# Kernel optimization log

Hardware: AMD Instinct MI355X
Metric: run time of the kernel (lower is better)

The kernel has to match this reference:

```python
import jax, jax.numpy as jnp
import numpy as np

N = 100000
E = 1600000
IN_F = 128
OUT_F = 32
HEADS = 6
NEG_SLOPE = 0.2


def setup_inputs() -> dict:
    key = jax.random.key(0)
    k1, k2, k3, k4, k5 = jax.random.split(key, 5)
    x = jax.random.normal(k1, (N, IN_F), dtype=jnp.float32)
    edge_index = jax.random.randint(k2, (2, E), 0, N, dtype=jnp.int64)
    # GATConv params (PyG layout): shared linear for src/dst, per-head attention vectors, bias
    glorot = lambda k, shape: jax.random.normal(k, shape, dtype=jnp.float32) * np.sqrt(2.0 / (shape[0] + shape[-1]))
    W = glorot(k3, (IN_F, HEADS * OUT_F))          # lin.weight^T
    att_src = glorot(k4, (HEADS, OUT_F)) * 0.1     # [H, C]
    att_dst = glorot(k5, (HEADS, OUT_F)) * 0.1
    bias = jnp.zeros((OUT_F,), dtype=jnp.float32)  # concat=False -> bias of size out_feature
    return {"x": x, "edge_index": edge_index, "W": W,
            "att_src": att_src, "att_dst": att_dst, "bias": bias}


def reference(x, edge_index, W, att_src, att_dst, bias):
    src, dst = edge_index[0], edge_index[1]
    # Linear projection to per-head features: [N, H, C]
    xp = (x @ W).reshape(N, HEADS, OUT_F)
    # Per-node attention logit halves: [N, H]
    a_s = jnp.einsum("nhc,hc->nh", xp, att_src)
    a_d = jnp.einsum("nhc,hc->nh", xp, att_dst)
    # Per-edge logits with LeakyReLU: [E, H]
    e = jax.nn.leaky_relu(a_s[src] + a_d[dst], negative_slope=NEG_SLOPE)
    # Segment softmax over edges grouped by destination node
    m = jax.ops.segment_max(e, dst, num_segments=N)            # [N, H]
    m = jnp.where(jnp.isfinite(m), m, 0.0)                     # empty segments -> -inf guard
    e = jnp.exp(e - m[dst])
    s = jax.ops.segment_sum(e, dst, num_segments=N)            # [N, H]
    alpha = e / (s[dst] + 1e-16)                               # [E, H]
    # Weighted scatter-add aggregation: [N, H, C]
    msg = xp[src] * alpha[:, :, None]
    out = jax.ops.segment_sum(msg, dst, num_segments=N)
    # concat=False -> mean over heads, add bias, then SELU
    out = out.mean(axis=1) + bias
    return jax.nn.selu(out)
```

## Files before the change

kernel.cpp:

```cpp
#include <hip/hip_runtime.h>


typedef __attribute__((ext_vector_type(8))) short short8;
typedef __attribute__((ext_vector_type(4))) float f32x4;

#define SK 136
#define SLOTS 48

__device__ __forceinline__ unsigned short f2bf(float f)
{
    unsigned int u = __float_as_uint(f);
    u = (u + 0x7fffu + ((u >> 16) & 1u)) >> 16;
    return (unsigned short)u;
}

__global__ __launch_bounds__(256) void k_prep(
    const float* __restrict__ W,
    const float* __restrict__ att_src, const float* __restrict__ att_dst,
    unsigned short* __restrict__ watT, unsigned short* __restrict__ WbT,
    int* __restrict__ deg, int N)
{
    int i = blockIdx.x * 256 + threadIdx.x;
    if (i < N) deg[i] = 0;
    if (i < 128 * 192) {
        int k = i / 192, c = i - k * 192;
        WbT[c * 128 + k] = f2bf(W[i]);
    }
    if (i < 128 * 16) {
        int k = i >> 4, c = i & 15;
        float v = 0.f;
        if (c < 12) {
            int h = c < 6 ? c : c - 6;
            const float* av = (c < 6 ? att_src : att_dst) + h * 32;
            const float* wr = W + k * 192 + h * 32;
            #pragma unroll
            for (int j = 0; j < 32; ++j) v = fmaf(wr[j], av[j], v);
        }
        watT[c * 128 + k] = f2bf(v);
    }
}

__global__ __launch_bounds__(384) void k_gd(
    const float* __restrict__ x, const unsigned short* __restrict__ WbT,
    const unsigned short* __restrict__ watT,
    unsigned char* __restrict__ xpb, float2* __restrict__ asc,
    float* __restrict__ a_d,
    const int* __restrict__ ei, int* __restrict__ deg, int* __restrict__ csr,
    int N, int E, int GB, int DB)
{
    __shared__ __align__(16) unsigned short xt[64 * SK];
    const int t   = threadIdx.x;
    const int bid = (int)blockIdx.x >> 1;

    if (blockIdx.x & 1) {
        if (bid >= DB) return;
        const int G = DB * 384;
        const int gid = bid * 384 + t;
        int s[4], d[4], r[4];
        #pragma unroll
        for (int k = 0; k < 4; ++k) {
            int e = gid + k * G;
            bool ok = e < E;
            int ec = ok ? e : 0;
            s[k] = ei[ec];
            d[k] = ei[E + ec];
            if (!ok) d[k] = -1;
        }
        #pragma unroll
        for (int k = 0; k < 4; ++k)
            r[k] = (d[k] >= 0) ? atomicAdd(&deg[d[k]], 1) : SLOTS;
        #pragma unroll
        for (int k = 0; k < 4; ++k)
            if (r[k] < SLOTS && d[k] >= 0) csr[d[k] * SLOTS + r[k]] = s[k];
        return;
    }

    if (bid >= GB) return;
    const int wave = t >> 6;
    const int lane = t & 63;
    const int ln   = lane & 15;
    const int q    = lane >> 4;
    const int n0   = bid * 64;
    const int cb   = wave * 32;

    {
        const float4* x4 = (const float4*)x;
        #pragma unroll
        for (int it = 0; it < 6; ++it) {
            int i = t + it * 384;
            if (i < 2048) {
                int row = i >> 5;
                int c4  = i & 31;
                int gr  = n0 + row;
                if (gr > N - 1) gr = N - 1;
                float4 f = x4[(size_t)gr * 32 + c4];
                unsigned int u0 = (unsigned int)f2bf(f.x) | ((unsigned int)f2bf(f.y) << 16);
                unsigned int u1 = (unsigned int)f2bf(f.z) | ((unsigned int)f2bf(f.w) << 16);
                *(uint2*)(xt + row * SK + c4 * 4) = make_uint2(u0, u1);
            }
        }
    }

    short8 bw[2][4];
    #pragma unroll
    for (int nt = 0; nt < 2; ++nt)
        #pragma unroll
        for (int kbi = 0; kbi < 4; ++kbi)
            bw[nt][kbi] = *(const short8*)(WbT + (cb + nt * 16 + ln) * 128
                                               + kbi * 32 + q * 8);
    short8 bwa[4];
    if (wave < 4) {
        #pragma unroll
        for (int kbi = 0; kbi < 4; ++kbi)
            bwa[kbi] = *(const short8*)(watT + ln * 128 + kbi * 32 + q * 8);
    }

    __syncthreads();

    f32x4 acc[4][2];
    #pragma unroll
    for (int mt = 0; mt < 4; ++mt)
        #pragma unroll
        for (int nt = 0; nt < 2; ++nt) acc[mt][nt] = (f32x4)0.f;

    #pragma unroll
    for (int kbi = 0; kbi < 4; ++kbi) {
        #pragma unroll
        for (int mt = 0; mt < 4; ++mt) {
            short8 av = *(const short8*)(xt + (mt * 16 + ln) * SK + kbi * 32 + q * 8);
            #pragma unroll
            for (int nt = 0; nt < 2; ++nt)
                acc[mt][nt] = __builtin_amdgcn_mfma_f32_16x16x32_bf16(
                    av, bw[nt][kbi], acc[mt][nt], 0, 0, 0);
        }
    }

    if (wave < 4) {
        f32x4 acca = (f32x4)0.f;
        #pragma unroll
        for (int kbi = 0; kbi < 4; ++kbi) {
            short8 av = *(const short8*)(xt + (wave * 16 + ln) * SK + kbi * 32 + q * 8);
            acca = __builtin_amdgcn_mfma_f32_16x16x32_bf16(av, bwa[kbi], acca, 0, 0, 0);
        }
        #pragma unroll
        for (int r = 0; r < 4; ++r) {
            int grow = n0 + wave * 16 + q * 4 + r;
            if (grow < N) {
                if (ln < 6)       asc[(size_t)grow * 6 + ln].x   = acca[r];
                else if (ln < 12) a_d[(size_t)grow * 6 + ln - 6] = acca[r];
            }
        }
    }

    #pragma unroll
    for (int mt = 0; mt < 4; ++mt) {
        #pragma unroll
        for (int r = 0; r < 4; ++r) {
            float m = fmaxf(fabsf(acc[mt][0][r]), fabsf(acc[mt][1][r]));
            #pragma unroll
            for (int d = 1; d <= 8; d <<= 1)
                m = fmaxf(m, __shfl_xor(m, d));
            int row  = mt * 16 + q * 4 + r;
            int grow = n0 + row;
            if (grow < N) {
                float inv = m > 0.f ? 127.f / m : 0.f;
                if (ln == 0) asc[(size_t)grow * 6 + wave].y = m * (1.f / 127.f);
                #pragma unroll
                for (int nt = 0; nt < 2; ++nt) {
                    int qv = (int)rintf(acc[mt][nt][r] * inv) + 128;
                    xpb[(size_t)grow * 192 + cb + nt * 16 + ln] = (unsigned char)qv;
                }
            }
        }
    }
}

__global__ __launch_bounds__(256) void k_agg(
    const unsigned char* __restrict__ xpb, const float2* __restrict__ asc,
    const float* __restrict__ a_d,
    const int* __restrict__ csr, const int* __restrict__ degv,
    const float* __restrict__ bias, float* __restrict__ out, int N)
{
    const int wid = threadIdx.x >> 6;
    const int l   = threadIdx.x & 63;
    const int n = blockIdx.x * 4 + wid;
    if (n >= N) return;

    int deg = degv[n];
    deg = deg < SLOTS ? deg : SLOTS;
    const int nb  = n * SLOTS;
    const int eh  = l >> 5;
    const int sl0 = l & 31;
    const int sl  = sl0 < 24 ? sl0 : 23;
    const int h   = sl >> 2;
    const unsigned slb = (unsigned)sl * 8u;
    const unsigned h8  = (unsigned)h * 8u;
    const char* __restrict__ xpB  = (const char*)xpb;
    const char* __restrict__ ascB = (const char*)asc;

    const float zd = a_d[(size_t)n * 6 + h];

    float a0 = 0.f, a1 = 0.f, a2 = 0.f, a3 = 0.f;
    float a4 = 0.f, a5 = 0.f, a6 = 0.f, a7 = 0.f;
    float se = 0.f, sevs = 0.f;

    int my3 = (l < deg && l < SLOTS) ? csr[nb + l] * 3 : 0;

    int i = 0;
    for (; i + 8 <= deg; i += 8) {
        unsigned s3[4]; float2 av[4]; uint2 xv[4];
        #pragma unroll
        for (int k = 0; k < 4; ++k) {
            s3[k] = (unsigned)__shfl(my3, i + 2 * k + eh);
            av[k] = *(const float2*)(ascB + s3[k] * 16u + h8);
        }
        #pragma unroll
        for (int k = 0; k < 4; ++k)
            xv[k] = *(const uint2*)(xpB + s3[k] * 64u + slb);
        #pragma unroll
        for (int k = 0; k < 4; ++k) {
            float z = av[k].x + zd;
            z = fmaxf(z, 0.2f * z);
            float ev = __expf(z);
            float evs = ev * av[k].y;
            unsigned va = xv[k].x, vb = xv[k].y;
            a0 = fmaf(evs, (float)(va & 0xffu), a0);
            a1 = fmaf(evs, (float)((va >> 8) & 0xffu), a1);
            a2 = fmaf(evs, (float)((va >> 16) & 0xffu), a2);
            a3 = fmaf(evs, (float)(va >> 24), a3);
            a4 = fmaf(evs, (float)(vb & 0xffu), a4);
            a5 = fmaf(evs, (float)((vb >> 8) & 0xffu), a5);
            a6 = fmaf(evs, (float)((vb >> 16) & 0xffu), a6);
            a7 = fmaf(evs, (float)(vb >> 24), a7);
            se += ev;
            sevs += evs;
        }
    }
    for (; i < deg; i += 2) {
        int e = i + eh;
        bool valid = e < deg;
        unsigned s3 = (unsigned)__shfl(my3, e < SLOTS ? e : 0);
        float2 av = *(const float2*)(ascB + s3 * 16u + h8);
        float z = av.x + zd;
        z = fmaxf(z, 0.2f * z);
        float ev = valid ? __expf(z) : 0.f;
        float evs = ev * av.y;
        uint2 xv = *(const uint2*)(xpB + s3 * 64u + slb);
        unsigned va = xv.x, vb = xv.y;
        a0 = fmaf(evs, (float)(va & 0xffu), a0);
        a1 = fmaf(evs, (float)((va >> 8) & 0xffu), a1);
        a2 = fmaf(evs, (float)((va >> 16) & 0xffu), a2);
        a3 = fmaf(evs, (float)(va >> 24), a3);
        a4 = fmaf(evs, (float)(vb & 0xffu), a4);
        a5 = fmaf(evs, (float)((vb >> 8) & 0xffu), a5);
        a6 = fmaf(evs, (float)((vb >> 16) & 0xffu), a6);
        a7 = fmaf(evs, (float)(vb >> 24), a7);
        se += ev;
        sevs += evs;
    }

    a0 += __shfl_xor(a0, 32); a1 += __shfl_xor(a1, 32);
    a2 += __shfl_xor(a2, 32); a3 += __shfl_xor(a3, 32);
    a4 += __shfl_xor(a4, 32); a5 += __shfl_xor(a5, 32);
    a6 += __shfl_xor(a6, 32); a7 += __shfl_xor(a7, 32);
    se += __shfl_xor(se, 32); sevs += __shfl_xor(sevs, 32);

    const float cor = 128.f * sevs;
    const float inv = 1.f / (se + 1e-16f);
    const bool act = (sl0 < 24);
    float v[8];
    float aa[8] = {a0, a1, a2, a3, a4, a5, a6, a7};
    #pragma unroll
    for (int j = 0; j < 8; ++j)
        v[j] = act ? (aa[j] - cor) * inv : 0.f;

    #pragma unroll
    for (int d = 4; d <= 16; d <<= 1) {
        #pragma unroll
        for (int j = 0; j < 8; ++j)
            v[j] += __shfl_down(v[j], d);
    }

    if (l < 4) {
        float4 b0 = ((const float4*)bias)[l * 2];
        float4 b1 = ((const float4*)bias)[l * 2 + 1];
        const float scs = 1.0507009873554805f, al = 1.6732632423543772f;
        float m[8] = {v[0] * (1.f / 6.f) + b0.x, v[1] * (1.f / 6.f) + b0.y,
                      v[2] * (1.f / 6.f) + b0.z, v[3] * (1.f / 6.f) + b0.w,
                      v[4] * (1.f / 6.f) + b1.x, v[5] * (1.f / 6.f) + b1.y,
                      v[6] * (1.f / 6.f) + b1.z, v[7] * (1.f / 6.f) + b1.w};
        #pragma unroll
        for (int k = 0; k < 8; ++k)
            m[k] = m[k] > 0.f ? scs * m[k] : scs * al * (__expf(m[k]) - 1.f);
        ((float4*)out)[(size_t)n * 8 + l * 2]     = make_float4(m[0], m[1], m[2], m[3]);
        ((float4*)out)[(size_t)n * 8 + l * 2 + 1] = make_float4(m[4], m[5], m[6], m[7]);
    }
}

extern "C" void kernel_launch(void* const* d_in, const int* in_sizes, int n_in,
                              void* d_out, int out_size, void* d_ws, size_t ws_size,
                              hipStream_t stream)
{
    const float* x       = (const float*)d_in[0];
    const int*   ei      = (const int*)d_in[1];
    const float* W       = (const float*)d_in[2];
    const float* att_src = (const float*)d_in[3];
    const float* att_dst = (const float*)d_in[4];
    const float* bias    = (const float*)d_in[5];
    float* out = (float*)d_out;

    const int N = in_sizes[0] / 128;
    const int E = in_sizes[1] / 2;
    const int GB = (N + 63) / 64;
    const int DB = (E + 4 * 384 - 1) / (4 * 384);
    const int MB = (GB > DB ? GB : DB) * 2;

    char* ws = (char*)d_ws;
    size_t o = 0;
    auto take = [&](size_t bytes) { size_t r = o; o = (o + bytes + 255) & ~(size_t)255; return r; };
    unsigned char* xpb = (unsigned char*)(ws + take((size_t)N * 192));
    float2* asc    = (float2*)(ws + take((size_t)N * 6 * 8));
    float*  a_d    = (float*) (ws + take((size_t)N * 6 * 4));
    int*    deg    = (int*)   (ws + take((size_t)N * 4));
    int*    csr    = (int*)   (ws + take((size_t)N * SLOTS * 4));
    unsigned short* watT = (unsigned short*)(ws + take((size_t)128 * 16 * 2));
    unsigned short* WbT  = (unsigned short*)(ws + take((size_t)128 * 192 * 2));
    (void)ws_size; (void)n_in; (void)out_size;

    int pg = (N + 255) / 256;
    k_prep<<<pg, 256, 0, stream>>>(W, att_src, att_dst, watT, WbT, deg, N);
    k_gd<<<MB, 384, 0, stream>>>(x, WbT, watT, xpb, asc, a_d,
                                 ei, deg, csr, N, E, GB, DB);
    k_agg<<<(N + 3) / 4, 256, 0, stream>>>(xpb, asc, a_d, csr, deg, bias, out, N);
}
```

Baseline: 280.8 us.

## Pre-convert x to bf16 and split edge placement from GEMM kernel

```diff
diff --git a/kernel.cpp b/kernel.cpp
--- a/kernel.cpp
+++ b/kernel.cpp
@@ -4,7 +4,6 @@
 typedef __attribute__((ext_vector_type(8))) short short8;
 typedef __attribute__((ext_vector_type(4))) float f32x4;
 
-#define SK 136
 #define SLOTS 48
 
 __device__ __forceinline__ unsigned short f2bf(float f)
@@ -14,20 +13,28 @@
     return (unsigned short)u;
 }
 
+__device__ __forceinline__ void gload_lds16(const void* g, void* l)
+{
+    __builtin_amdgcn_global_load_lds(
+        (const __attribute__((address_space(1))) unsigned int*)g,
+        (__attribute__((address_space(3))) unsigned int*)l, 16, 0, 0);
+}
+
 __global__ __launch_bounds__(256) void k_prep(
     const float* __restrict__ W,
     const float* __restrict__ att_src, const float* __restrict__ att_dst,
+    const float* __restrict__ x,
     unsigned short* __restrict__ watT, unsigned short* __restrict__ WbT,
-    int* __restrict__ deg, int N)
-{
-    int i = blockIdx.x * 256 + threadIdx.x;
-    if (i < N) deg[i] = 0;
-    if (i < 128 * 192) {
-        int k = i / 192, c = i - k * 192;
-        WbT[c * 128 + k] = f2bf(W[i]);
-    }
-    if (i < 128 * 16) {
-        int k = i >> 4, c = i & 15;
+    unsigned short* __restrict__ xb, int* __restrict__ deg, int N)
+{
+    int gid = blockIdx.x * 256 + threadIdx.x;
+    if (gid < N) deg[gid] = 0;
+    if (gid < 128 * 192) {
+        int k = gid / 192, c = gid - k * 192;
+        WbT[c * 128 + k] = f2bf(W[gid]);
+    }
+    if (gid < 128 * 16) {
+        int k = gid >> 4, c = gid & 15;
         float v = 0.f;
         if (c < 12) {
             int h = c < 6 ? c : c - 6;
@@ -38,66 +45,66 @@
         }
         watT[c * 128 + k] = f2bf(v);
     }
-}
-
-__global__ __launch_bounds__(384) void k_gd(
-    const float* __restrict__ x, const unsigned short* __restrict__ WbT,
+    if (gid < N * 16) {
+        const float4* x4 = (const float4*)x;
+        float4 f0 = x4[(size_t)gid * 2];
+        float4 f1 = x4[(size_t)gid * 2 + 1];
+        uint4 u;
+        u.x = (unsigned)f2bf(f0.x) | ((unsigned)f2bf(f0.y) << 16);
+        u.y = (unsigned)f2bf(f0.z) | ((unsigned)f2bf(f0.w) << 16);
+        u.z = (unsigned)f2bf(f1.x) | ((unsigned)f2bf(f1.y) << 16);
+        u.w = (unsigned)f2bf(f1.z) | ((unsigned)f2bf(f1.w) << 16);
+        ((uint4*)xb)[gid] = u;
+    }
+}
+
+__global__ __launch_bounds__(256) void k_place(
+    const int* __restrict__ ei, int* __restrict__ deg, int* __restrict__ csr,
+    int E, int DB)
+{
+    const int G = DB * 256;
+    const int gid = blockIdx.x * 256 + threadIdx.x;
+    int s[4], d[4], r[4];
+    #pragma unroll
+    for (int k = 0; k < 4; ++k) {
+        int e = gid + k * G;
+        bool ok = e < E;
+        int ec = ok ? e : 0;
+        s[k] = ei[ec];
+        d[k] = ei[E + ec];
+        if (!ok) d[k] = -1;
+    }
+    #pragma unroll
+    for (int k = 0; k < 4; ++k)
+        r[k] = (d[k] >= 0) ? atomicAdd(&deg[d[k]], 1) : SLOTS;
+    #pragma unroll
+    for (int k = 0; k < 4; ++k)
+        if (r[k] < SLOTS && d[k] >= 0) csr[d[k] * SLOTS + r[k]] = s[k];
+}
+
+__global__ __launch_bounds__(384) void k_gemm(
+    const unsigned short* __restrict__ xb,
+    const unsigned short* __restrict__ WbT,
     const unsigned short* __restrict__ watT,
     unsigned char* __restrict__ xpb, float2* __restrict__ asc,
-    float* __restrict__ a_d,
-    const int* __restrict__ ei, int* __restrict__ deg, int* __restrict__ csr,
-    int N, int E, int GB, int DB)
-{
-    __shared__ __align__(16) unsigned short xt[64 * SK];
-    const int t   = threadIdx.x;
-    const int bid = (int)blockIdx.x >> 1;
-
-    if (blockIdx.x & 1) {
-        if (bid >= DB) return;
-        const int G = DB * 384;
-        const int gid = bid * 384 + t;
-        int s[4], d[4], r[4];
-        #pragma unroll
-        for (int k = 0; k < 4; ++k) {
-            int e = gid + k * G;
-            bool ok = e < E;
-            int ec = ok ? e : 0;
-            s[k] = ei[ec];
-            d[k] = ei[E + ec];
-            if (!ok) d[k] = -1;
-        }
-        #pragma unroll
-        for (int k = 0; k < 4; ++k)
-            r[k] = (d[k] >= 0) ? atomicAdd(&deg[d[k]], 1) : SLOTS;
-        #pragma unroll
-        for (int k = 0; k < 4; ++k)
-            if (r[k] < SLOTS && d[k] >= 0) csr[d[k] * SLOTS + r[k]] = s[k];
-        return;
-    }
-
-    if (bid >= GB) return;
+    float* __restrict__ a_d, int N)
+{
+    __shared__ __align__(16) unsigned short xt[64 * 128];
+    const int t    = threadIdx.x;
     const int wave = t >> 6;
     const int lane = t & 63;
     const int ln   = lane & 15;
     const int q    = lane >> 4;
-    const int n0   = bid * 64;
+    const int n0   = (int)blockIdx.x * 64;
     const int cb   = wave * 32;
 
-    {
-        const float4* x4 = (const float4*)x;
-        #pragma unroll
-        for (int it = 0; it < 6; ++it) {
-            int i = t + it * 384;
-            if (i < 2048) {
-                int row = i >> 5;
-                int c4  = i & 31;
-                int gr  = n0 + row;
-                if (gr > N - 1) gr = N - 1;
-                float4 f = x4[(size_t)gr * 32 + c4];
-                unsigned int u0 = (unsigned int)f2bf(f.x) | ((unsigned int)f2bf(f.y) << 16);
-                unsigned int u1 = (unsigned int)f2bf(f.z) | ((unsigned int)f2bf(f.w) << 16);
-                *(uint2*)(xt + row * SK + c4 * 4) = make_uint2(u0, u1);
-            }
+    #pragma unroll
+    for (int it = 0; it < 3; ++it) {
+        int idx = t + it * 384;
+        if (idx < 1024) {
+            int r  = idx >> 4, sl = idx & 15;
+            int gs = sl ^ ((r & 7) << 1);
+            gload_lds16(xb + (size_t)(n0 + r) * 128 + gs * 8, xt + idx * 8);
         }
     }
 
@@ -123,11 +130,13 @@
         #pragma unroll
         for (int nt = 0; nt < 2; ++nt) acc[mt][nt] = (f32x4)0.f;
 
+    const int swz = (ln & 7) << 1;
     #pragma unroll
     for (int kbi = 0; kbi < 4; ++kbi) {
+        const int ps = (kbi * 4 + q) ^ swz;
         #pragma unroll
         for (int mt = 0; mt < 4; ++mt) {
-            short8 av = *(const short8*)(xt + (mt * 16 + ln) * SK + kbi * 32 + q * 8);
+            short8 av = *(const short8*)(xt + (mt * 16 + ln) * 128 + ps * 8);
             #pragma unroll
             for (int nt = 0; nt < 2; ++nt)
                 acc[mt][nt] = __builtin_amdgcn_mfma_f32_16x16x32_bf16(
@@ -139,7 +148,8 @@
         f32x4 acca = (f32x4)0.f;
         #pragma unroll
         for (int kbi = 0; kbi < 4; ++kbi) {
-            short8 av = *(const short8*)(xt + (wave * 16 + ln) * SK + kbi * 32 + q * 8);
+            const int ps = (kbi * 4 + q) ^ swz;
+            short8 av = *(const short8*)(xt + (wave * 16 + ln) * 128 + ps * 8);
             acca = __builtin_amdgcn_mfma_f32_16x16x32_bf16(av, bwa[kbi], acca, 0, 0, 0);
         }
         #pragma unroll
@@ -312,8 +322,7 @@
     const int N = in_sizes[0] / 128;
     const int E = in_sizes[1] / 2;
     const int GB = (N + 63) / 64;
-    const int DB = (E + 4 * 384 - 1) / (4 * 384);
-    const int MB = (GB > DB ? GB : DB) * 2;
+    const int DB = (E + 4 * 256 - 1) / (4 * 256);
 
     char* ws = (char*)d_ws;
     size_t o = 0;
@@ -325,11 +334,12 @@
     int*    csr    = (int*)   (ws + take((size_t)N * SLOTS * 4));
     unsigned short* watT = (unsigned short*)(ws + take((size_t)128 * 16 * 2));
     unsigned short* WbT  = (unsigned short*)(ws + take((size_t)128 * 192 * 2));
+    unsigned short* xb   = (unsigned short*)(ws + take((size_t)GB * 64 * 128 * 2));
     (void)ws_size; (void)n_in; (void)out_size;
 
-    int pg = (N + 255) / 256;
-    k_prep<<<pg, 256, 0, stream>>>(W, att_src, att_dst, watT, WbT, deg, N);
-    k_gd<<<MB, 384, 0, stream>>>(x, WbT, watT, xpb, asc, a_d,
-                                 ei, deg, csr, N, E, GB, DB);
+    int pg = (N * 16 + 255) / 256;
+    k_prep<<<pg, 256, 0, stream>>>(W, att_src, att_dst, x, watT, WbT, xb, deg, N);
+    k_place<<<DB, 256, 0, stream>>>(ei, deg, csr, E, DB);
+    k_gemm<<<GB, 384, 0, stream>>>(xb, WbT, watT, xpb, asc, a_d, N);
     k_agg<<<(N + 3) / 4, 256, 0, stream>>>(xpb, asc, a_d, csr, deg, bias, out, N);
 }
```

Result: slower. 365.6 us (+30.2%).

## Partition CSR build by destination range per XCD with dynamic chunk queues

Applied to the files above, without the earlier changes.

```diff
diff --git a/kernel.cpp b/kernel.cpp
--- a/kernel.cpp
+++ b/kernel.cpp
@@ -6,6 +6,7 @@
 
 #define SK 136
 #define SLOTS 48
+#define PCH 1536
 
 __device__ __forceinline__ unsigned short f2bf(float f)
 {
@@ -18,10 +19,11 @@
     const float* __restrict__ W,
     const float* __restrict__ att_src, const float* __restrict__ att_dst,
     unsigned short* __restrict__ watT, unsigned short* __restrict__ WbT,
-    int* __restrict__ deg, int N)
+    int* __restrict__ deg, int* __restrict__ qctr, int N)
 {
     int i = blockIdx.x * 256 + threadIdx.x;
     if (i < N) deg[i] = 0;
+    if (i < 128) qctr[i] = 0;
     if (i < 128 * 192) {
         int k = i / 192, c = i - k * 192;
         WbT[c * 128 + k] = f2bf(W[i]);
@@ -46,32 +48,43 @@
     unsigned char* __restrict__ xpb, float2* __restrict__ asc,
     float* __restrict__ a_d,
     const int* __restrict__ ei, int* __restrict__ deg, int* __restrict__ csr,
-    int N, int E, int GB, int DB)
+    int* __restrict__ qctr,
+    int N, int E, int GB, int NCH, int SH)
 {
     __shared__ __align__(16) unsigned short xt[64 * SK];
+    __shared__ int qs;
     const int t   = threadIdx.x;
     const int bid = (int)blockIdx.x >> 1;
 
     if (blockIdx.x & 1) {
-        if (bid >= DB) return;
-        const int G = DB * 384;
-        const int gid = bid * 384 + t;
-        int s[4], d[4], r[4];
-        #pragma unroll
-        for (int k = 0; k < 4; ++k) {
-            int e = gid + k * G;
-            bool ok = e < E;
-            int ec = ok ? e : 0;
-            s[k] = ei[ec];
-            d[k] = ei[E + ec];
-            if (!ok) d[k] = -1;
-        }
-        #pragma unroll
-        for (int k = 0; k < 4; ++k)
-            r[k] = (d[k] >= 0) ? atomicAdd(&deg[d[k]], 1) : SLOTS;
-        #pragma unroll
-        for (int k = 0; k < 4; ++k)
-            if (r[k] < SLOTS && d[k] >= 0) csr[d[k] * SLOTS + r[k]] = s[k];
+        int xcd;
+        asm volatile("s_getreg_b32 %0, hwreg(HW_REG_XCC_ID)" : "=s"(xcd));
+        xcd &= 7;
+        for (int so = 0; so < 8; ++so) {
+            const int s   = (xcd + so) & 7;
+            const int dlo = s * SH;
+            const int dhi = (dlo + SH < N) ? dlo + SH : N;
+            while (true) {
+                __syncthreads();
+                if (t == 0) qs = atomicAdd(&qctr[s * 16], 1);
+                __syncthreads();
+                const int c = qs;
+                if (c >= NCH) break;
+                const int base = c * PCH + t;
+                #pragma unroll
+                for (int k = 0; k < 4; ++k) {
+                    int e = base + k * 384;
+                    if (e < E) {
+                        int d = ei[E + e];
+                        int sv = ei[e];
+                        if (d >= dlo && d < dhi) {
+                            int r = atomicAdd(&deg[d], 1);
+                            if (r < SLOTS) csr[d * SLOTS + r] = sv;
+                        }
+                    }
+                }
+            }
+        }
         return;
     }
 
@@ -311,9 +324,10 @@
 
     const int N = in_sizes[0] / 128;
     const int E = in_sizes[1] / 2;
-    const int GB = (N + 63) / 64;
-    const int DB = (E + 4 * 384 - 1) / (4 * 384);
-    const int MB = (GB > DB ? GB : DB) * 2;
+    const int GB  = (N + 63) / 64;
+    const int NCH = (E + PCH - 1) / PCH;
+    const int SH  = (N + 7) / 8;
+    const int MB  = GB * 2;
 
     char* ws = (char*)d_ws;
     size_t o = 0;
@@ -323,13 +337,14 @@
     float*  a_d    = (float*) (ws + take((size_t)N * 6 * 4));
     int*    deg    = (int*)   (ws + take((size_t)N * 4));
     int*    csr    = (int*)   (ws + take((size_t)N * SLOTS * 4));
+    int*    qctr   = (int*)   (ws + take((size_t)128 * 4));
     unsigned short* watT = (unsigned short*)(ws + take((size_t)128 * 16 * 2));
     unsigned short* WbT  = (unsigned short*)(ws + take((size_t)128 * 192 * 2));
     (void)ws_size; (void)n_in; (void)out_size;
 
     int pg = (N + 255) / 256;
-    k_prep<<<pg, 256, 0, stream>>>(W, att_src, att_dst, watT, WbT, deg, N);
+    k_prep<<<pg, 256, 0, stream>>>(W, att_src, att_dst, watT, WbT, deg, qctr, N);
     k_gd<<<MB, 384, 0, stream>>>(x, WbT, watT, xpb, asc, a_d,
-                                 ei, deg, csr, N, E, GB, DB);
+                                 ei, deg, csr, qctr, N, E, GB, NCH, SH);
     k_agg<<<(N + 3) / 4, 256, 0, stream>>>(xpb, asc, a_d, csr, deg, bias, out, N);
 }
```

New measurement: 355.1 us. 1.26x slower.
